# Performance work log

Hardware: AMD Instinct MI355X
Metric: run time of the kernel (lower is better)

The kernel has to match this reference:

```python
import jax, jax.numpy as jnp
import numpy as np

N = 100000
LS = (0, 1, 2)
MULS = (128, 64, 32)   # multiplicities of 0e,1o,2e in input1 / mid / out
MUL_Y = 64             # input2 = 64x0e (pure scalars)
DIM_X = sum(m * (2 * l + 1) for m, l in zip(MULS, LS))  # 480


def _split_irreps(x):
    # x: (N, 480) -> list of (N, mul, 2l+1) blocks
    parts, off = [], 0
    for m, l in zip(MULS, LS):
        d = m * (2 * l + 1)
        parts.append(x[:, off:off + d].reshape(-1, m, 2 * l + 1))
        off += d
    return parts


def setup_inputs() -> dict:
    key = jax.random.key(0)
    ks = jax.random.split(key, 8)
    inp = {
        "x": jax.random.normal(ks[0], (N, DIM_X), jnp.float32),
        "y": jax.random.normal(ks[1], (N, MUL_Y), jnp.float32),
    }
    for i, m in enumerate(MULS):
        # e3nn internal weights ~ N(0,1); path normalization applied in forward
        inp[f"W_tp{i}"] = jax.random.normal(ks[2 + i], (m, MUL_Y, m), jnp.float32)
        inp[f"W_lin{i}"] = jax.random.normal(ks[5 + i], (m, m), jnp.float32)
    return inp


def reference(x, y, W_tp0, W_tp1, W_tp2, W_lin0, W_lin1, W_lin2):
    W_tp = (W_tp0, W_tp1, W_tp2)
    W_lin = (W_lin0, W_lin1, W_lin2)
    xs = _split_irreps(x)
    outs = []
    for m, l, Wt, Wl, xl in zip(MULS, LS, W_tp, W_lin, xs):
        # e3nn 'uvw' path with scalar (0e) second input:
        #   CG(l,0,l)[m1,0,mo] = delta / sqrt(2l+1)
        #   path_weight = sqrt(ir_out.dim / (mul1*mul2)) = sqrt((2l+1)/(m*MUL_Y))
        # net coefficient = 1 / sqrt(m * MUL_Y)
        c_tp = float(1.0 / np.sqrt(m * MUL_Y))
        mid = c_tp * jnp.einsum('uvw,num,nv->nwm', Wt, xl, y)  # (N, m, 2l+1)
        # o3.Linear: single path per irrep, weight 1/sqrt(fan_in), fan_in = m
        c_lin = float(1.0 / np.sqrt(m))
        out = c_lin * jnp.einsum('uw,num->nwm', Wl, mid)       # (N, m, 2l+1)
        outs.append(out.reshape(-1, m * (2 * l + 1)))
    return jnp.concatenate(outs, axis=-1)  # (N, 480)
```

## Files before the change

### kernel.cpp

```cpp
#include <hip/hip_runtime.h>


typedef _Float16 f16x8 __attribute__((ext_vector_type(8)));
typedef _Float16 h2    __attribute__((ext_vector_type(2)));
typedef float    f32x4 __attribute__((ext_vector_type(4)));

__device__ __forceinline__ void gload_lds16(const void* g, void* l) {
    __builtin_amdgcn_global_load_lds(
        (const __attribute__((address_space(1))) unsigned*)g,
        (__attribute__((address_space(3))) unsigned*)l, 16, 0, 0);
}

template<int M, int NT>
__global__ void pack_b(const float* __restrict__ Wt, const float* __restrict__ Wl,
                       _Float16* __restrict__ Bp) {
    const int gid = blockIdx.x * 256 + threadIdx.x;
    const int total = M * 64 * M / 2;
    if (gid >= total) return;
    const int w_ = gid & (M - 1);
    const int uvp = gid / M;
    const float4* wtA = (const float4*)(Wt + (size_t)(2 * uvp) * M);
    const float4* wtB = (const float4*)(Wt + (size_t)(2 * uvp + 1) * M);
    float a0 = 0.f, a1 = 0.f;
    #pragma unroll 4
    for (int w = 0; w < M; w += 4) {
        float4 tA = wtA[w >> 2], tB = wtB[w >> 2];
        float l0 = Wl[(w + 0) * M + w_], l1 = Wl[(w + 1) * M + w_];
        float l2 = Wl[(w + 2) * M + w_], l3 = Wl[(w + 3) * M + w_];
        a0 += tA.x * l0 + tA.y * l1 + tA.z * l2 + tA.w * l3;
        a1 += tB.x * l0 + tB.y * l1 + tB.z * l2 + tB.w * l3;
    }
    #pragma unroll
    for (int t = 0; t < 2; ++t) {
        const int uv = 2 * uvp + t;
        const int u = uv >> 6, v = uv & 63;
        const int vh = v >> 5, vv = v & 31, quad = vv >> 3, j = vv & 7;
        const int kc = u * 2 + vh, nt = w_ >> 4, lane = quad * 16 + (w_ & 15);
        Bp[((size_t)(kc * NT + nt) * 64 + lane) * 8 + j] = (_Float16)(t ? a1 : a0);
    }
}

template<int M, int NCOMP, int XOFF, int NT, int KC, int MT>
__device__ __forceinline__ void tp_block(char* smem, int wg,
    const float* __restrict__ x, const float* __restrict__ y,
    const _Float16* __restrict__ Bp, float* __restrict__ out, int Rtot, float cscale)
{
    constexpr int WAVES_M = 4, WAVES_N = 2;
    constexpr int WM = MT / (WAVES_M * 16);
    constexpr int WN = NT / WAVES_N;
    constexpr int UC = KC / 2;
    constexpr int XU = 16;
    constexpr int XS = 20;
    constexpr int KTOT = 2 * M;
    constexpr int NCHUNK = KTOT / KC;
    constexpr int CPS = XU / UC;
    constexpr int NSLAB = M / XU;
    constexpr int BCH = KC * NT * 1024;
    constexpr int XSL = MT * XS * 4;
    constexpr int NS_T = MT / NCOMP + 2;
    constexpr int XE = NS_T * XU * NCOMP;
    constexpr int XITER = (XE + 511) / 512;

    char* bb0 = smem;
    char* bb1 = smem + BCH;
    char* xb0 = smem + 2 * BCH;
    char* xb1 = smem + 2 * BCH + XSL;

    const int tid = threadIdx.x;
    const int lane = tid & 63;
    const int wv = tid >> 6;
    const int wvn = wv & 1;
    const int wvm = wv >> 1;
    const int l15 = lane & 15;
    const int quad = lane >> 4;
    const int r0 = wg * MT;
    const int s0 = r0 / NCOMP;
    const int k0 = r0 - s0 * NCOMP;

    float xt[XITER];
    auto xld = [&](int slab) {
        const int ub = slab * XU;
        #pragma unroll
        for (int i = 0; i < XITER; ++i) {
            const int p = tid + i * 512;
            float v = 0.f;
            if (p < XE) {
                const int sl = p / (XU * NCOMP);
                const int fo = p - sl * (XU * NCOMP);
                const int ul = fo / NCOMP;
                const int k  = fo - ul * NCOMP;
                const int rl = sl * NCOMP + k - k0;
                if (rl >= 0 && rl < MT && (r0 + rl) < Rtot)
                    v = x[(size_t)(s0 + sl) * 480 + XOFF + (ub + ul) * NCOMP + k];
            }
            xt[i] = v;
        }
    };
    auto xwr = [&](char* xd) {
        #pragma unroll
        for (int i = 0; i < XITER; ++i) {
            const int p = tid + i * 512;
            if (p < XE) {
                const int sl = p / (XU * NCOMP);
                const int fo = p - sl * (XU * NCOMP);
                const int ul = fo / NCOMP;
                const int k  = fo - ul * NCOMP;
                const int rl = sl * NCOMP + k - k0;
                if (rl >= 0 && rl < MT) {
                    union { _Float16 h; unsigned short u; } cv; cv.h = (_Float16)xt[i];
                    const unsigned pp = (unsigned)cv.u | ((unsigned)cv.u << 16);
                    *(unsigned*)(xd + (unsigned)((rl * XS + ul) << 2)) = pp;
                }
            }
        }
    };
    auto stageB = [&](int c, char* bd) {
        const char* gs = (const char*)Bp + (size_t)c * BCH + wv * 2048 + lane * 16;
        char* ld = bd + wv * 2048;
        gload_lds16(gs, ld);
        gload_lds16(gs + 1024, ld + 1024);
    };

    int rowf[WM];
    union YH { f16x8 v; h2 h[4]; };
    YH yh[2][WM];
    #pragma unroll
    for (int f = 0; f < WM; ++f) {
        rowf[f] = wvm * (WM * 16) + f * 16 + l15;
        const int Rg = r0 + rowf[f];
        const int sf = (Rg < Rtot) ? (int)((unsigned)Rg / NCOMP) : 0;
        #pragma unroll
        for (int vh = 0; vh < 2; ++vh) {
            const float4* yp = (const float4*)(y + (size_t)sf * 64 + vh * 32 + quad * 8);
            const float4 a = yp[0], b = yp[1];
            union { f16x8 v; _Float16 e[8]; } t;
            t.e[0] = (_Float16)a.x; t.e[1] = (_Float16)a.y;
            t.e[2] = (_Float16)a.z; t.e[3] = (_Float16)a.w;
            t.e[4] = (_Float16)b.x; t.e[5] = (_Float16)b.y;
            t.e[6] = (_Float16)b.z; t.e[7] = (_Float16)b.w;
            yh[vh][f].v = t.v;
        }
    }

    f32x4 acc[WM][WN];
    #pragma unroll
    for (int f = 0; f < WM; ++f)
        #pragma unroll
        for (int g = 0; g < WN; ++g) acc[f][g] = f32x4{0.f, 0.f, 0.f, 0.f};

    xld(0);
    stageB(0, bb0);
    xwr(xb0);
    __syncthreads();

    int bcur = 0, xcur = 0;
    #pragma unroll 1
    for (int c = 0; c < NCHUNK; ++c) {
        if (c + 1 < NCHUNK) stageB(c + 1, bcur ? bb0 : bb1);
        const int cm = c & (CPS - 1);
        const int sl1 = c / CPS + 1;
        if (cm == 0 && sl1 < NSLAB) xld(sl1);

        const char* bs = bcur ? bb1 : bb0;
        const char* xs = xcur ? xb1 : xb0;
        const int uoff = cm * UC;

        uint4 xv[WM];
        #pragma unroll
        for (int f = 0; f < WM; ++f) {
            const char* xa = xs + (unsigned)((rowf[f] * XS + uoff) << 2);
            if constexpr (UC == 1)      { xv[f].x = *(const unsigned*)xa; }
            else if constexpr (UC == 2) { const uint2 t = *(const uint2*)xa; xv[f].x = t.x; xv[f].y = t.y; }
            else                        { xv[f] = *(const uint4*)xa; }
        }
        #pragma unroll
        for (int kl = 0; kl < KC; ++kl) {
            const int vh = kl & 1, uo = kl >> 1;
            f16x8 bg[WN];
            #pragma unroll
            for (int g = 0; g < WN; ++g)
                bg[g] = *(const f16x8*)(bs + (unsigned)((kl * NT + wvn * WN + g) << 10) + lane * 16);
            f16x8 af[WM];
            #pragma unroll
            for (int f = 0; f < WM; ++f) {
                const unsigned px = (uo == 0) ? xv[f].x : (uo == 1) ? xv[f].y
                                  : (uo == 2) ? xv[f].z : xv[f].w;
                union { unsigned u; h2 h; } xb2; xb2.u = px;
                union { f16x8 v; h2 h[4]; } a_;
                #pragma unroll
                for (int q = 0; q < 4; ++q) a_.h[q] = xb2.h * yh[vh][f].h[q];
                af[f] = a_.v;
            }
            #pragma unroll
            for (int f = 0; f < WM; ++f)
                #pragma unroll
                for (int g = 0; g < WN; ++g)
                    acc[f][g] = __builtin_amdgcn_mfma_f32_16x16x32_f16(af[f], bg[g], acc[f][g], 0, 0, 0);
        }
        if (cm == CPS - 1 && sl1 < NSLAB) xwr(xcur ? xb0 : xb1);
        __syncthreads();
        bcur ^= 1;
        if (cm == CPS - 1) xcur ^= 1;
    }

    #pragma unroll
    for (int f = 0; f < WM; ++f) {
        #pragma unroll
        for (int g = 0; g < WN; ++g) {
            const int col = (wvn * WN + g) * 16 + l15;
            #pragma unroll
            for (int r = 0; r < 4; ++r) {
                const int R = r0 + wvm * (WM * 16) + f * 16 + quad * 4 + r;
                if (R < Rtot) {
                    const int s = (int)((unsigned)R / NCOMP);
                    const int k = R - s * NCOMP;
                    out[(size_t)s * 480 + XOFF + col * NCOMP + k] = acc[f][g][r] * cscale;
                }
            }
        }
    }
}

__global__ __launch_bounds__(512, 2)
void tp_main(const float* __restrict__ x, const float* __restrict__ y,
             const _Float16* __restrict__ B0, const _Float16* __restrict__ B1,
             const _Float16* __restrict__ B2, float* __restrict__ out,
             int R0, int R1, int R2, int G0, int G1)
{
    __shared__ char smem[114688];
    const int b = blockIdx.x;
    if (b < G0)            tp_block<128, 1,   0, 8, 2, 384>(smem, b,           x, y, B0, out, R0, 1.f / 1024.f);
    else if (b < G0 + G1)  tp_block< 64, 3, 128, 4, 4, 512>(smem, b - G0,      x, y, B1, out, R1, 1.f / 512.f);
    else                   tp_block< 32, 5, 320, 2, 8, 512>(smem, b - G0 - G1, x, y, B2, out, R2, 1.f / 256.f);
}

extern "C" void kernel_launch(void* const* d_in, const int* in_sizes, int n_in,
                              void* d_out, int out_size, void* d_ws, size_t ws_size,
                              hipStream_t stream) {
    const float* x   = (const float*)d_in[0];
    const float* y   = (const float*)d_in[1];
    const float* Wt0 = (const float*)d_in[2];
    const float* Wl0 = (const float*)d_in[3];
    const float* Wt1 = (const float*)d_in[4];
    const float* Wl1 = (const float*)d_in[5];
    const float* Wt2 = (const float*)d_in[6];
    const float* Wl2 = (const float*)d_in[7];
    float* out = (float*)d_out;

    const int Ns = in_sizes[0] / 480;

    _Float16* B0 = (_Float16*)d_ws;
    _Float16* B1 = B0 + 8192 * 128;
    _Float16* B2 = B1 + 4096 * 64;

    pack_b<128, 8><<<(128 * 64 * 128 / 2 + 255) / 256, 256, 0, stream>>>(Wt0, Wl0, B0);
    pack_b< 64, 4><<<( 64 * 64 *  64 / 2 + 255) / 256, 256, 0, stream>>>(Wt1, Wl1, B1);
    pack_b< 32, 2><<<( 32 * 64 *  32 / 2 + 255) / 256, 256, 0, stream>>>(Wt2, Wl2, B2);

    const int R0 = Ns, R1 = Ns * 3, R2 = Ns * 5;
    const int G0 = (R0 + 383) / 384;
    const int G1 = (R1 + 511) / 512;
    const int G2 = (R2 + 511) / 512;
    tp_main<<<G0 + G1 + G2, 512, 0, stream>>>(x, y, B0, B1, B2, out, R0, R1, R2, G0, G1);
}
```

Baseline: 740.0 us.

## Reorder K dimension v-half-major to halve y registers and shrink x slab

Packed B is reordered so the reduction runs over all u for the first half of v, then all u for the second half. Each thread therefore holds y fragments for only one v-half at a time and reloads the other half midway through the loop, roughly halving the y register footprint. The x slab shrinks from 16 to 8 u-columns and is cycled twice through the slabs, which lowers LDS use from 112KB to 80KB. The aim is better occupancy or less register pressure, at the cost of loading and converting each x slab twice and an extra y load mid-loop.

```diff
diff --git a/kernel.cpp b/kernel.cpp
--- a/kernel.cpp
+++ b/kernel.cpp
@@ -35,7 +35,7 @@
         const int uv = 2 * uvp + t;
         const int u = uv >> 6, v = uv & 63;
         const int vh = v >> 5, vv = v & 31, quad = vv >> 3, j = vv & 7;
-        const int kc = u * 2 + vh, nt = w_ >> 4, lane = quad * 16 + (w_ & 15);
+        const int kc = vh * M + u, nt = w_ >> 4, lane = quad * 16 + (w_ & 15);
         Bp[((size_t)(kc * NT + nt) * 64 + lane) * 8 + j] = (_Float16)(t ? a1 : a0);
     }
 }
@@ -45,21 +45,22 @@
     const float* __restrict__ x, const float* __restrict__ y,
     const _Float16* __restrict__ Bp, float* __restrict__ out, int Rtot, float cscale)
 {
-    constexpr int WAVES_M = 4, WAVES_N = 2;
-    constexpr int WM = MT / (WAVES_M * 16);
-    constexpr int WN = NT / WAVES_N;
-    constexpr int UC = KC / 2;
-    constexpr int XU = 16;
-    constexpr int XS = 20;
+    constexpr int WM = MT / 64;
+    constexpr int WN = NT / 2;
+    constexpr int XU = 8;
+    constexpr int XS = 12;
     constexpr int KTOT = 2 * M;
     constexpr int NCHUNK = KTOT / KC;
-    constexpr int CPS = XU / UC;
+    constexpr int HC = NCHUNK / 2;
+    constexpr int CPS = XU / KC;
     constexpr int NSLAB = M / XU;
     constexpr int BCH = KC * NT * 1024;
     constexpr int XSL = MT * XS * 4;
     constexpr int NS_T = MT / NCOMP + 2;
     constexpr int XE = NS_T * XU * NCOMP;
     constexpr int XITER = (XE + 511) / 512;
+    constexpr int RW = (KC < 4) ? KC : 4;
+    constexpr int NRW = KC / RW;
 
     char* bb0 = smem;
     char* bb1 = smem + BCH;
@@ -121,26 +122,28 @@
         gload_lds16(gs + 1024, ld + 1024);
     };
 
-    int rowf[WM];
-    union YH { f16x8 v; h2 h[4]; };
-    YH yh[2][WM];
+    int rowf[WM], sfr[WM];
     #pragma unroll
     for (int f = 0; f < WM; ++f) {
         rowf[f] = wvm * (WM * 16) + f * 16 + l15;
         const int Rg = r0 + rowf[f];
-        const int sf = (Rg < Rtot) ? (int)((unsigned)Rg / NCOMP) : 0;
-        #pragma unroll
-        for (int vh = 0; vh < 2; ++vh) {
-            const float4* yp = (const float4*)(y + (size_t)sf * 64 + vh * 32 + quad * 8);
+        sfr[f] = (Rg < Rtot) ? (int)((unsigned)Rg / NCOMP) : 0;
+    }
+    union YH { f16x8 v; h2 h[4]; };
+    YH yh[WM];
+    auto loady = [&](int vh) {
+        #pragma unroll
+        for (int f = 0; f < WM; ++f) {
+            const float4* yp = (const float4*)(y + (size_t)sfr[f] * 64 + vh * 32 + quad * 8);
             const float4 a = yp[0], b = yp[1];
             union { f16x8 v; _Float16 e[8]; } t;
             t.e[0] = (_Float16)a.x; t.e[1] = (_Float16)a.y;
             t.e[2] = (_Float16)a.z; t.e[3] = (_Float16)a.w;
             t.e[4] = (_Float16)b.x; t.e[5] = (_Float16)b.y;
             t.e[6] = (_Float16)b.z; t.e[7] = (_Float16)b.w;
-            yh[vh][f].v = t.v;
-        }
-    }
+            yh[f].v = t.v;
+        }
+    };
 
     f32x4 acc[WM][WN];
     #pragma unroll
@@ -151,53 +154,57 @@
     xld(0);
     stageB(0, bb0);
     xwr(xb0);
+    loady(0);
     __syncthreads();
 
-    int bcur = 0, xcur = 0;
+    int bcur = 0, xcur = 0, nsl = 1;
     #pragma unroll 1
     for (int c = 0; c < NCHUNK; ++c) {
         if (c + 1 < NCHUNK) stageB(c + 1, bcur ? bb0 : bb1);
         const int cm = c & (CPS - 1);
-        const int sl1 = c / CPS + 1;
-        if (cm == 0 && sl1 < NSLAB) xld(sl1);
+        if (cm == 0 && c + CPS < NCHUNK) { xld(nsl & (NSLAB - 1)); ++nsl; }
+        if (c == HC) loady(1);
 
         const char* bs = bcur ? bb1 : bb0;
         const char* xs = xcur ? xb1 : xb0;
-        const int uoff = cm * UC;
-
-        uint4 xv[WM];
-        #pragma unroll
-        for (int f = 0; f < WM; ++f) {
-            const char* xa = xs + (unsigned)((rowf[f] * XS + uoff) << 2);
-            if constexpr (UC == 1)      { xv[f].x = *(const unsigned*)xa; }
-            else if constexpr (UC == 2) { const uint2 t = *(const uint2*)xa; xv[f].x = t.x; xv[f].y = t.y; }
-            else                        { xv[f] = *(const uint4*)xa; }
-        }
-        #pragma unroll
-        for (int kl = 0; kl < KC; ++kl) {
-            const int vh = kl & 1, uo = kl >> 1;
-            f16x8 bg[WN];
-            #pragma unroll
-            for (int g = 0; g < WN; ++g)
-                bg[g] = *(const f16x8*)(bs + (unsigned)((kl * NT + wvn * WN + g) << 10) + lane * 16);
-            f16x8 af[WM];
+
+        #pragma unroll
+        for (int rw = 0; rw < NRW; ++rw) {
+            unsigned xv[WM][RW];
             #pragma unroll
             for (int f = 0; f < WM; ++f) {
-                const unsigned px = (uo == 0) ? xv[f].x : (uo == 1) ? xv[f].y
-                                  : (uo == 2) ? xv[f].z : xv[f].w;
-                union { unsigned u; h2 h; } xb2; xb2.u = px;
-                union { f16x8 v; h2 h[4]; } a_;
-                #pragma unroll
-                for (int q = 0; q < 4; ++q) a_.h[q] = xb2.h * yh[vh][f].h[q];
-                af[f] = a_.v;
+                const char* xa = xs + (unsigned)((rowf[f] * XS + cm * KC + rw * RW) << 2);
+                if constexpr (RW == 2) {
+                    const uint2 t = *(const uint2*)xa; xv[f][0] = t.x; xv[f][1] = t.y;
+                } else {
+                    const uint4 t = *(const uint4*)xa;
+                    xv[f][0] = t.x; xv[f][1] = t.y; xv[f][2] = t.z; xv[f][3] = t.w;
+                }
             }
             #pragma unroll
-            for (int f = 0; f < WM; ++f)
+            for (int kk = 0; kk < RW; ++kk) {
+                const int kl = rw * RW + kk;
+                f16x8 bg[WN];
                 #pragma unroll
                 for (int g = 0; g < WN; ++g)
-                    acc[f][g] = __builtin_amdgcn_mfma_f32_16x16x32_f16(af[f], bg[g], acc[f][g], 0, 0, 0);
-        }
-        if (cm == CPS - 1 && sl1 < NSLAB) xwr(xcur ? xb0 : xb1);
+                    bg[g] = *(const f16x8*)(bs + (unsigned)(((kl * NT + wvn * WN + g) << 10) + lane * 16));
+                f16x8 af[WM];
+                #pragma unroll
+                for (int f = 0; f < WM; ++f) {
+                    union { unsigned u; h2 h; } xb2; xb2.u = xv[f][kk];
+                    union { f16x8 v; h2 h[4]; } a_;
+                    #pragma unroll
+                    for (int q = 0; q < 4; ++q) a_.h[q] = xb2.h * yh[f].h[q];
+                    af[f] = a_.v;
+                }
+                #pragma unroll
+                for (int f = 0; f < WM; ++f)
+                    #pragma unroll
+                    for (int g = 0; g < WN; ++g)
+                        acc[f][g] = __builtin_amdgcn_mfma_f32_16x16x32_f16(af[f], bg[g], acc[f][g], 0, 0, 0);
+            }
+        }
+        if (cm == CPS - 1 && c + 1 < NCHUNK) xwr(xcur ? xb0 : xb1);
         __syncthreads();
         bcur ^= 1;
         if (cm == CPS - 1) xcur ^= 1;
@@ -227,7 +234,7 @@
              const _Float16* __restrict__ B2, float* __restrict__ out,
              int R0, int R1, int R2, int G0, int G1)
 {
-    __shared__ char smem[114688];
+    __shared__ char smem[81920];
     const int b = blockIdx.x;
     if (b < G0)            tp_block<128, 1,   0, 8, 2, 384>(smem, b,           x, y, B0, out, R0, 1.f / 1024.f);
     else if (b < G0 + G1)  tp_block< 64, 3, 128, 4, 4, 512>(smem, b - G0,      x, y, B1, out, R1, 1.f / 512.f);
```

Measured after the change: 736.4 us. Within noise of the previous version (-0.5%).
